# Kernel tuning notes

Hardware: AMD Instinct MI355X
Metric: run time of the kernel (lower is better)

## Reference

```python
import jax, jax.numpy as jnp
import numpy as np

HEADS = 8
HEAD_DIM = 64
GROUPS = 32
EPS = 1e-5


def setup_inputs() -> dict:
    key = jax.random.key(0)
    ks = jax.random.split(key, 8)
    B, C, H, W = 16, 256, 32, 32
    TD = 1024
    inner = HEADS * HEAD_DIM
    return {
        "x": jax.random.normal(ks[0], (B, C, H, W), jnp.float32),
        "embedding": jax.random.normal(ks[1], (B, TD), jnp.float32),
        "norm_w": jnp.ones((C,), jnp.float32),
        "norm_b": jnp.zeros((C,), jnp.float32),
        "in_w": jax.random.normal(ks[2], (3 * inner, C), jnp.float32) * (1.0 / np.sqrt(C)),
        "in_b": jnp.zeros((3 * inner,), jnp.float32),
        "out_w": jax.random.normal(ks[3], (C, inner), jnp.float32) * (1.0 / np.sqrt(inner)),
        "out_b": jnp.zeros((C,), jnp.float32),
        "emb_w": jax.random.normal(ks[4], (C, TD), jnp.float32) * (1.0 / np.sqrt(TD)),
        "emb_b": jnp.zeros((C,), jnp.float32),
    }


def reference(x, embedding, norm_w, norm_b, in_w, in_b, out_w, out_b, emb_w, emb_b):
    b, c, h, w = x.shape
    scale = 1.0 / np.sqrt(HEAD_DIM)
    # GroupNorm over (C//G, H, W) per group
    xg = x.reshape(b, GROUPS, -1)
    mean = xg.mean(-1, keepdims=True)
    var = xg.var(-1, keepdims=True)
    xn = ((xg - mean) * jax.lax.rsqrt(var + EPS)).reshape(b, c, h, w)
    xn = xn * norm_w[:, None, None] + norm_b[:, None, None]
    # 1x1 conv QKV projection: [b, 3*inner, h, w]
    qkv = jnp.einsum('oc,bchw->bohw', in_w, xn) + in_b[:, None, None]
    q, k, v = jnp.split(qkv, 3, axis=1)
    # [b, heads, head_dim, hw]
    q = q.reshape(b, HEADS, HEAD_DIM, h * w)
    k = k.reshape(b, HEADS, HEAD_DIM, h * w)
    v = v.reshape(b, HEADS, HEAD_DIM, h * w)
    attn = jax.nn.softmax(jnp.einsum('bhcm,bhcn->bhmn', q, k) * scale, axis=-1)
    o = jnp.einsum('bhmn,bhcn->bhcm', attn, v)  # [b,h,c,hw]
    o = o.reshape(b, HEADS * HEAD_DIM, h, w)
    out = jnp.einsum('oc,bchw->bohw', out_w, o) + out_b[:, None, None]
    emb = embedding @ emb_w.T + emb_b  # [b, C]
    return out * emb[:, :, None, None] + x
```

## Files before the change

kernel.cpp:

```cpp
#include <hip/hip_runtime.h>

#define DEV __device__ __forceinline__

typedef _Float16 f16;
typedef _Float16 f16x8 __attribute__((ext_vector_type(8)));
typedef _Float16 f16x4 __attribute__((ext_vector_type(4)));
typedef float f32x4 __attribute__((ext_vector_type(4)));

static constexpr int NB = 16;
static constexpr int NC = 256;
static constexpr int HW = 1024;
static constexpr int NG = 32;
static constexpr int CPG = 8;
static constexpr int NH = 8;
static constexpr int HD = 64;
static constexpr int INNER = 512;
static constexpr int TD = 1024;

DEV f32x4 mfma16(f16x8 a, f16x8 b, f32x4 c) {
    return __builtin_amdgcn_mfma_f32_16x16x32_f16(a, b, c, 0, 0, 0);
}

__global__ void gn_stats_k(const float* __restrict__ x, float* __restrict__ stats) {
    int bg = blockIdx.x;
    const float4* p = reinterpret_cast<const float4*>(x) + (size_t)bg * (CPG * HW / 4);
    float s = 0.f, ss = 0.f;
    for (int i = threadIdx.x; i < CPG * HW / 4; i += 256) {
        float4 v = p[i];
        s  += v.x + v.y + v.z + v.w;
        ss += v.x * v.x + v.y * v.y + v.z * v.z + v.w * v.w;
    }
    #pragma unroll
    for (int o = 32; o > 0; o >>= 1) {
        s  += __shfl_xor(s, o);
        ss += __shfl_xor(ss, o);
    }
    __shared__ float rs[4], rss[4];
    int wid = threadIdx.x >> 6;
    if ((threadIdx.x & 63) == 0) { rs[wid] = s; rss[wid] = ss; }
    __syncthreads();
    if (threadIdx.x == 0) {
        s  = rs[0] + rs[1] + rs[2] + rs[3];
        ss = rss[0] + rss[1] + rss[2] + rss[3];
        const float inv_n = 1.f / (float)(CPG * HW);
        float mean = s * inv_n;
        float var  = ss * inv_n - mean * mean;
        stats[bg * 2]     = mean;
        stats[bg * 2 + 1] = rsqrtf(var + 1e-5f);
    }
}

__global__ void gn_apply_k(const float* __restrict__ x, const float* __restrict__ stats,
                           const float* __restrict__ nw, const float* __restrict__ nb,
                           f16* __restrict__ xnT) {
    int b = blockIdx.y;
    int m = blockIdx.x * 256 + threadIdx.x;
    const float* xb = x + (size_t)b * NC * HW + m;
    f16* op = xnT + ((size_t)b * HW + m) * NC;
    for (int c0 = 0; c0 < NC; c0 += 4) {
        f16x4 h;
        #pragma unroll
        for (int j = 0; j < 4; ++j) {
            int c = c0 + j;
            float mean = stats[(b * NG + (c >> 3)) * 2];
            float rstd = stats[(b * NG + (c >> 3)) * 2 + 1];
            float v = xb[(size_t)c * HW];
            h[j] = (f16)(((v - mean) * rstd) * nw[c] + nb[c]);
        }
        *reinterpret_cast<f16x4*>(op + c0) = h;
    }
}

__global__ void conv_w_k(const float* __restrict__ a, const float* __restrict__ bw,
                         f16* __restrict__ wa, f16* __restrict__ wb) {
    int i = blockIdx.x * 256 + threadIdx.x;
    const int N1 = 3 * INNER * NC / 4;
    float4 v;
    f16* dst;
    if (i < N1) { v = reinterpret_cast<const float4*>(a)[i];      dst = wa + (size_t)i * 4; }
    else        { v = reinterpret_cast<const float4*>(bw)[i - N1]; dst = wb + (size_t)(i - N1) * 4; }
    f16x4 h4 = {(f16)v.x, (f16)v.y, (f16)v.z, (f16)v.w};
    *reinterpret_cast<f16x4*>(dst) = h4;
}

__global__ __launch_bounds__(256) void gemm_qkv_k(
        const f16* __restrict__ wA, const f16* __restrict__ xnT,
        const float* __restrict__ bias,
        f16* __restrict__ qT, f16* __restrict__ kT, f16* __restrict__ vv) {
    int b  = blockIdx.z;
    int o0 = blockIdx.x * 128;
    int m0 = blockIdx.y * 128;
    int wid  = threadIdx.x >> 6;
    int lane = threadIdx.x & 63;
    int wr = (wid >> 1) * 64, wc = (wid & 1) * 64;
    int lr = lane & 15, lg = lane >> 4;

    const f16* A  = wA  + (size_t)(o0 + wr + lr) * NC + lg * 8;
    const f16* Bp = xnT + ((size_t)b * HW + m0 + wc + lr) * NC + lg * 8;

    const f32x4 fzero = {0.f, 0.f, 0.f, 0.f};
    f32x4 acc[4][4];
    #pragma unroll
    for (int i = 0; i < 4; ++i) {
        #pragma unroll
        for (int j = 0; j < 4; ++j) acc[i][j] = fzero;
    }

    for (int k0 = 0; k0 < NC; k0 += 32) {
        f16x8 af[4], bf[4];
        #pragma unroll
        for (int i = 0; i < 4; ++i)
            af[i] = *reinterpret_cast<const f16x8*>(A + (size_t)i * 16 * NC + k0);
        #pragma unroll
        for (int j = 0; j < 4; ++j)
            bf[j] = *reinterpret_cast<const f16x8*>(Bp + (size_t)j * 16 * NC + k0);
        #pragma unroll
        for (int i = 0; i < 4; ++i) {
            #pragma unroll
            for (int j = 0; j < 4; ++j)
                acc[i][j] = mfma16(af[i], bf[j], acc[i][j]);
        }
    }

    #pragma unroll
    for (int i = 0; i < 4; ++i) {
        int ob = o0 + wr + i * 16 + lg * 4;
        #pragma unroll
        for (int j = 0; j < 4; ++j) {
            int m = m0 + wc + j * 16 + lr;
            float v0 = acc[i][j][0] + bias[ob];
            float v1 = acc[i][j][1] + bias[ob + 1];
            float v2 = acc[i][j][2] + bias[ob + 2];
            float v3 = acc[i][j][3] + bias[ob + 3];
            if (ob < INNER) {
                int h = ob >> 6, c = ob & 63;
                f16x4 pk = {(f16)v0, (f16)v1, (f16)v2, (f16)v3};
                *reinterpret_cast<f16x4*>(qT + (((size_t)(b * NH + h) * HW + m) * HD + c)) = pk;
            } else if (ob < 2 * INNER) {
                int oo = ob - INNER;
                int h = oo >> 6, c = oo & 63;
                f16x4 pk = {(f16)v0, (f16)v1, (f16)v2, (f16)v3};
                *reinterpret_cast<f16x4*>(kT + (((size_t)(b * NH + h) * HW + m) * HD + c)) = pk;
            } else {
                int oo = ob - 2 * INNER;
                int h = oo >> 6, c = oo & 63;
                f16* vp = vv + ((size_t)(b * NH + h) * HD + c) * HW + m;
                vp[0]      = (f16)v0;
                vp[HW]     = (f16)v1;
                vp[2 * HW] = (f16)v2;
                vp[3 * HW] = (f16)v3;
            }
        }
    }
}

__global__ void emb_gemm_k(const float* __restrict__ e, const float* __restrict__ ew,
                           const float* __restrict__ eb, float* __restrict__ embS) {
    int b = blockIdx.y;
    int co = blockIdx.x * 4 + (threadIdx.x >> 6);
    int lane = threadIdx.x & 63;
    const float4* ep = reinterpret_cast<const float4*>(e + (size_t)b * TD);
    const float4* wp = reinterpret_cast<const float4*>(ew + (size_t)co * TD);
    float s = 0.f;
    for (int t = lane; t < TD / 4; t += 64) {
        float4 a = ep[t], w = wp[t];
        s += a.x * w.x + a.y * w.y + a.z * w.z + a.w * w.w;
    }
    #pragma unroll
    for (int o = 32; o > 0; o >>= 1) s += __shfl_xor(s, o);
    if (lane == 0) embS[b * NC + co] = s + eb[co];
}

DEV void load_kv(const f16* __restrict__ kp, const f16* __restrict__ vp,
                 int n0, int lr, int lg, f16x8 (&kf)[2][2], f16x8 (&vf)[4]) {
    #pragma unroll
    for (int kt = 0; kt < 2; ++kt)
        #pragma unroll
        for (int ks2 = 0; ks2 < 2; ++ks2)
            kf[kt][ks2] = *reinterpret_cast<const f16x8*>(
                kp + (size_t)(n0 + kt * 16 + lr) * HD + ks2 * 32 + lg * 8);
    #pragma unroll
    for (int dt = 0; dt < 4; ++dt)
        vf[dt] = *reinterpret_cast<const f16x8*>(
            vp + (size_t)(dt * 16 + lr) * HW + n0 + lg * 8);
}

DEV void attn_tile(const f16x8 (&kf)[2][2], const f16x8 (&vf)[4],
                   const f16x8 (&qf)[4][2],
                   f32x4 (&oa)[4][4], float (&mr)[4], float (&lsl)[4],
                   f16 (&pl)[16][40], int lr, int lg) {
    const float sl = 0.125f * 1.44269504088896f;
    const float THR = 11.0f;
    const f32x4 fzero = {0.f, 0.f, 0.f, 0.f};
    #pragma unroll
    for (int qt = 0; qt < 4; ++qt) {
        f32x4 sc0 = fzero, sc1 = fzero;
        __builtin_amdgcn_s_setprio(1);
        sc0 = mfma16(kf[0][0], qf[qt][0], sc0);
        sc0 = mfma16(kf[0][1], qf[qt][1], sc0);
        sc1 = mfma16(kf[1][0], qf[qt][0], sc1);
        sc1 = mfma16(kf[1][1], qf[qt][1], sc1);
        __builtin_amdgcn_s_setprio(0);

        float a0 = fmaxf(fmaxf(sc0[0], sc0[1]), fmaxf(sc0[2], sc0[3]));
        float a1 = fmaxf(fmaxf(sc1[0], sc1[1]), fmaxf(sc1[2], sc1[3]));
        float pmax = fmaxf(a0, a1) * sl;
        if (__any(pmax - mr[qt] > THR)) {
            float pm = pmax;
            pm = fmaxf(pm, __shfl_xor(pm, 16));
            pm = fmaxf(pm, __shfl_xor(pm, 32));
            float mn = fmaxf(mr[qt], pm);
            float f = exp2f(mr[qt] - mn);
            mr[qt] = mn;
            lsl[qt] *= f;
            #pragma unroll
            for (int dt = 0; dt < 4; ++dt)
                #pragma unroll
                for (int r = 0; r < 4; ++r) oa[qt][dt][r] *= f;
        }
        float p[8];
        #pragma unroll
        for (int r = 0; r < 4; ++r) p[r]     = exp2f(fmaf(sc0[r], sl, -mr[qt]));
        #pragma unroll
        for (int r = 0; r < 4; ++r) p[4 + r] = exp2f(fmaf(sc1[r], sl, -mr[qt]));
        lsl[qt] += ((p[0] + p[1]) + (p[2] + p[3])) + ((p[4] + p[5]) + (p[6] + p[7]));

        f16x4 w0 = {(f16)p[0], (f16)p[1], (f16)p[2], (f16)p[3]};
        f16x4 w1 = {(f16)p[4], (f16)p[5], (f16)p[6], (f16)p[7]};
        *reinterpret_cast<f16x4*>(&pl[lr][lg * 4])      = w0;
        *reinterpret_cast<f16x4*>(&pl[lr][16 + lg * 4]) = w1;
        f16x8 pf = *reinterpret_cast<const f16x8*>(&pl[lr][lg * 8]);

        __builtin_amdgcn_s_setprio(1);
        #pragma unroll
        for (int dt = 0; dt < 4; ++dt)
            oa[qt][dt] = mfma16(vf[dt], pf, oa[qt][dt]);
        __builtin_amdgcn_s_setprio(0);
    }
}

__global__ __launch_bounds__(256) void attn_k(
        const f16* __restrict__ qT, const f16* __restrict__ kT, const f16* __restrict__ vv,
        f16* __restrict__ oT) {
    int u = ((blockIdx.x & 7) << 6) | (blockIdx.x >> 3);
    int bh = u >> 2;
    int mt = u & 3;
    int b = bh >> 3, h = bh & 7;
    int wid = threadIdx.x >> 6;
    int lane = threadIdx.x & 63;
    int lr = lane & 15, lg = lane >> 4;
    int mw = mt * 256 + wid * 64;

    const f16* qp = qT + (size_t)bh * HW * HD;
    const f16* kp = kT + (size_t)bh * HW * HD;
    const f16* vp = vv + (size_t)bh * HD * HW;

    __shared__ __align__(16) f16 pl[4][16][40];

    f16x8 qf[4][2];
    #pragma unroll
    for (int qt = 0; qt < 4; ++qt)
        #pragma unroll
        for (int ks2 = 0; ks2 < 2; ++ks2)
            qf[qt][ks2] = *reinterpret_cast<const f16x8*>(
                qp + (size_t)(mw + qt * 16 + lr) * HD + ks2 * 32 + lg * 8);

    const f32x4 fzero = {0.f, 0.f, 0.f, 0.f};
    f32x4 oa[4][4];
    #pragma unroll
    for (int qt = 0; qt < 4; ++qt)
        #pragma unroll
        for (int dt = 0; dt < 4; ++dt) oa[qt][dt] = fzero;
    float mr[4]  = {-1e30f, -1e30f, -1e30f, -1e30f};
    float lsl[4] = {0.f, 0.f, 0.f, 0.f};

    f16x8 kfA[2][2], vfA[4], kfB[2][2], vfB[4];
    load_kv(kp, vp, 0, lr, lg, kfA, vfA);
    for (int n0 = 0; n0 < HW; n0 += 64) {
        load_kv(kp, vp, n0 + 32, lr, lg, kfB, vfB);
        attn_tile(kfA, vfA, qf, oa, mr, lsl, pl[wid], lr, lg);
        if (n0 + 64 < HW) load_kv(kp, vp, n0 + 64, lr, lg, kfA, vfA);
        attn_tile(kfB, vfB, qf, oa, mr, lsl, pl[wid], lr, lg);
    }

    #pragma unroll
    for (int qt = 0; qt < 4; ++qt) {
        float t = lsl[qt];
        t += __shfl_xor(t, 16);
        t += __shfl_xor(t, 32);
        float inv = 1.f / t;
        int m = mw + qt * 16 + lr;
        f16* op = oT + ((size_t)b * HW + m) * INNER + h * HD;
        #pragma unroll
        for (int dt = 0; dt < 4; ++dt) {
            f16x4 o4;
            #pragma unroll
            for (int r = 0; r < 4; ++r) o4[r] = (f16)(oa[qt][dt][r] * inv);
            *reinterpret_cast<f16x4*>(op + dt * 16 + lg * 4) = o4;
        }
    }
}

__global__ __launch_bounds__(256) void gemm_out_k(
        const f16* __restrict__ wA, const f16* __restrict__ oT,
        const float* __restrict__ bias, const float* __restrict__ embS,
        const float* __restrict__ x, float* __restrict__ out) {
    int b  = blockIdx.z;
    int o0 = blockIdx.x * 128;
    int m0 = blockIdx.y * 128;
    int wid  = threadIdx.x >> 6;
    int lane = threadIdx.x & 63;
    int wr = (wid >> 1) * 64, wc = (wid & 1) * 64;
    int lr = lane & 15, lg = lane >> 4;

    const f16* A  = wA + (size_t)(o0 + wr + lr) * INNER + lg * 8;
    const f16* Bp = oT + ((size_t)b * HW + m0 + wc + lr) * INNER + lg * 8;

    const f32x4 fzero = {0.f, 0.f, 0.f, 0.f};
    f32x4 acc[4][4];
    #pragma unroll
    for (int i = 0; i < 4; ++i) {
        #pragma unroll
        for (int j = 0; j < 4; ++j) acc[i][j] = fzero;
    }

    for (int k0 = 0; k0 < INNER; k0 += 32) {
        f16x8 af[4], bf[4];
        #pragma unroll
        for (int i = 0; i < 4; ++i)
            af[i] = *reinterpret_cast<const f16x8*>(A + (size_t)i * 16 * INNER + k0);
        #pragma unroll
        for (int j = 0; j < 4; ++j)
            bf[j] = *reinterpret_cast<const f16x8*>(Bp + (size_t)j * 16 * INNER + k0);
        #pragma unroll
        for (int i = 0; i < 4; ++i) {
            #pragma unroll
            for (int j = 0; j < 4; ++j)
                acc[i][j] = mfma16(af[i], bf[j], acc[i][j]);
        }
    }

    #pragma unroll
    for (int i = 0; i < 4; ++i) {
        int ob = o0 + wr + i * 16 + lg * 4;
        #pragma unroll
        for (int j = 0; j < 4; ++j) {
            int m = m0 + wc + j * 16 + lr;
            #pragma unroll
            for (int r = 0; r < 4; ++r) {
                int o = ob + r;
                size_t idx = ((size_t)b * NC + o) * HW + m;
                out[idx] = (acc[i][j][r] + bias[o]) * embS[b * NC + o] + x[idx];
            }
        }
    }
}

extern "C" void kernel_launch(void* const* d_in, const int* in_sizes, int n_in,
                              void* d_out, int out_size, void* d_ws, size_t ws_size,
                              hipStream_t stream) {
    const float* x     = (const float*)d_in[0];
    const float* emb   = (const float*)d_in[1];
    const float* nw    = (const float*)d_in[2];
    const float* nbi   = (const float*)d_in[3];
    const float* in_w  = (const float*)d_in[4];
    const float* in_b  = (const float*)d_in[5];
    const float* out_w = (const float*)d_in[6];
    const float* out_b = (const float*)d_in[7];
    const float* emb_w = (const float*)d_in[8];
    const float* emb_b = (const float*)d_in[9];

    char* p = (char*)d_ws;
    f16* xnT   = (f16*)p;   p += (size_t)NB * HW * NC * 2;
    f16* w_in  = (f16*)p;   p += (size_t)3 * INNER * NC * 2;
    f16* w_out = (f16*)p;   p += (size_t)NC * INNER * 2;
    float* stats = (float*)p; p += (size_t)NB * NG * 2 * 4;
    float* embS  = (float*)p; p += (size_t)NB * NC * 4;
    f16* qT = (f16*)p;      p += (size_t)NB * NH * HW * HD * 2;
    f16* kT = (f16*)p;      p += (size_t)NB * NH * HW * HD * 2;
    f16* vv = (f16*)p;      p += (size_t)NB * NH * HW * HD * 2;
    f16* oT = (f16*)p;

    gn_stats_k<<<NB * NG, 256, 0, stream>>>(x, stats);
    gn_apply_k<<<dim3(HW / 256, NB), 256, 0, stream>>>(x, stats, nw, nbi, xnT);
    conv_w_k<<<512, 256, 0, stream>>>(in_w, out_w, w_in, w_out);
    gemm_qkv_k<<<dim3(12, 8, NB), 256, 0, stream>>>(w_in, xnT, in_b, qT, kT, vv);
    emb_gemm_k<<<dim3(NC / 4, NB), 256, 0, stream>>>(emb, emb_w, emb_b, embS);
    attn_k<<<512, 256, 0, stream>>>(qT, kT, vv, oT);
    gemm_out_k<<<dim3(NC / 128, HW / 128, NB), 256, 0, stream>>>(w_out, oT, out_b, embS, x, (float*)d_out);
}
```

Baseline: 178.4 us.

## Fuse prep kernels, fold softmax scale into K, remap GEMM grids

Merges the GroupNorm stats, weight conversion and embedding GEMM into one launch to cut launch overhead and let independent work overlap. Folds the softmax scale and log2e into K when the QKV GEMM writes it, which removes a multiply per score in attention, and packs probabilities with cvt_pkrtz. The QKV and output GEMMs get a 1D grid with a swizzled block order for better cache locality. The output GEMM uses smaller 64-row tiles for more blocks, and gn_apply is reorganised to write 8-wide vectors across more blocks. K is now stored pre-scaled in fp16, which slightly changes rounding.

```diff
diff --git a/kernel.cpp b/kernel.cpp
--- a/kernel.cpp
+++ b/kernel.cpp
@@ -6,6 +6,7 @@
 typedef _Float16 f16x8 __attribute__((ext_vector_type(8)));
 typedef _Float16 f16x4 __attribute__((ext_vector_type(4)));
 typedef float f32x4 __attribute__((ext_vector_type(4)));
+typedef unsigned int u32;
 
 static constexpr int NB = 16;
 static constexpr int NC = 256;
@@ -21,32 +22,69 @@
     return __builtin_amdgcn_mfma_f32_16x16x32_f16(a, b, c, 0, 0, 0);
 }
 
-__global__ void gn_stats_k(const float* __restrict__ x, float* __restrict__ stats) {
-    int bg = blockIdx.x;
-    const float4* p = reinterpret_cast<const float4*>(x) + (size_t)bg * (CPG * HW / 4);
-    float s = 0.f, ss = 0.f;
-    for (int i = threadIdx.x; i < CPG * HW / 4; i += 256) {
-        float4 v = p[i];
-        s  += v.x + v.y + v.z + v.w;
-        ss += v.x * v.x + v.y * v.y + v.z * v.z + v.w * v.w;
-    }
-    #pragma unroll
-    for (int o = 32; o > 0; o >>= 1) {
-        s  += __shfl_xor(s, o);
-        ss += __shfl_xor(ss, o);
-    }
-    __shared__ float rs[4], rss[4];
-    int wid = threadIdx.x >> 6;
-    if ((threadIdx.x & 63) == 0) { rs[wid] = s; rss[wid] = ss; }
-    __syncthreads();
-    if (threadIdx.x == 0) {
-        s  = rs[0] + rs[1] + rs[2] + rs[3];
-        ss = rss[0] + rss[1] + rss[2] + rss[3];
-        const float inv_n = 1.f / (float)(CPG * HW);
-        float mean = s * inv_n;
-        float var  = ss * inv_n - mean * mean;
-        stats[bg * 2]     = mean;
-        stats[bg * 2 + 1] = rsqrtf(var + 1e-5f);
+DEV u32 pk2(float a, float b) {
+    auto c = __builtin_amdgcn_cvt_pkrtz(a, b);
+    return __builtin_bit_cast(u32, c);
+}
+struct u32x2 { u32 a, b; };
+
+__global__ void prep_k(const float* __restrict__ x, float* __restrict__ stats,
+                       const float* __restrict__ in_w, const float* __restrict__ out_w,
+                       f16* __restrict__ w_in, f16* __restrict__ w_out,
+                       const float* __restrict__ e, const float* __restrict__ ew,
+                       const float* __restrict__ eb, float* __restrict__ embS) {
+    int bid = blockIdx.x;
+    if (bid < NB * NG) {
+        int bg = bid;
+        const float4* p = reinterpret_cast<const float4*>(x) + (size_t)bg * (CPG * HW / 4);
+        float s = 0.f, ss = 0.f;
+        for (int i = threadIdx.x; i < CPG * HW / 4; i += 256) {
+            float4 v = p[i];
+            s  += v.x + v.y + v.z + v.w;
+            ss += v.x * v.x + v.y * v.y + v.z * v.z + v.w * v.w;
+        }
+        #pragma unroll
+        for (int o = 32; o > 0; o >>= 1) {
+            s  += __shfl_xor(s, o);
+            ss += __shfl_xor(ss, o);
+        }
+        __shared__ float rs[4], rss[4];
+        int wid = threadIdx.x >> 6;
+        if ((threadIdx.x & 63) == 0) { rs[wid] = s; rss[wid] = ss; }
+        __syncthreads();
+        if (threadIdx.x == 0) {
+            s  = rs[0] + rs[1] + rs[2] + rs[3];
+            ss = rss[0] + rss[1] + rss[2] + rss[3];
+            const float inv_n = 1.f / (float)(CPG * HW);
+            float mean = s * inv_n;
+            float var  = ss * inv_n - mean * mean;
+            stats[bg * 2]     = mean;
+            stats[bg * 2 + 1] = rsqrtf(var + 1e-5f);
+        }
+    } else if (bid < NB * NG + 512) {
+        int i = (bid - NB * NG) * 256 + threadIdx.x;
+        const int N1 = 3 * INNER * NC / 4;
+        float4 v;
+        f16* dst;
+        if (i < N1) { v = reinterpret_cast<const float4*>(in_w)[i];       dst = w_in + (size_t)i * 4; }
+        else        { v = reinterpret_cast<const float4*>(out_w)[i - N1]; dst = w_out + (size_t)(i - N1) * 4; }
+        f16x4 h4 = {(f16)v.x, (f16)v.y, (f16)v.z, (f16)v.w};
+        *reinterpret_cast<f16x4*>(dst) = h4;
+    } else {
+        int u = bid - (NB * NG + 512);
+        int b = u >> 6;
+        int co = ((u & 63) << 2) + (threadIdx.x >> 6);
+        int lane = threadIdx.x & 63;
+        const float4* ep = reinterpret_cast<const float4*>(e + (size_t)b * TD);
+        const float4* wp = reinterpret_cast<const float4*>(ew + (size_t)co * TD);
+        float s = 0.f;
+        for (int t = lane; t < TD / 4; t += 64) {
+            float4 a = ep[t], w = wp[t];
+            s += a.x * w.x + a.y * w.y + a.z * w.z + a.w * w.w;
+        }
+        #pragma unroll
+        for (int o = 32; o > 0; o >>= 1) s += __shfl_xor(s, o);
+        if (lane == 0) embS[b * NC + co] = s + eb[co];
     }
 }
 
@@ -54,42 +92,36 @@
                            const float* __restrict__ nw, const float* __restrict__ nb,
                            f16* __restrict__ xnT) {
     int b = blockIdx.y;
-    int m = blockIdx.x * 256 + threadIdx.x;
+    int m = blockIdx.x * 64 + (threadIdx.x & 63);
+    int c0 = (threadIdx.x >> 6) * 64;
     const float* xb = x + (size_t)b * NC * HW + m;
-    f16* op = xnT + ((size_t)b * HW + m) * NC;
-    for (int c0 = 0; c0 < NC; c0 += 4) {
-        f16x4 h;
-        #pragma unroll
-        for (int j = 0; j < 4; ++j) {
-            int c = c0 + j;
-            float mean = stats[(b * NG + (c >> 3)) * 2];
-            float rstd = stats[(b * NG + (c >> 3)) * 2 + 1];
+    f16* op = xnT + ((size_t)b * HW + m) * NC + c0;
+    #pragma unroll
+    for (int cc = 0; cc < 64; cc += 8) {
+        int cg = c0 + cc;
+        float mean = stats[(b * NG + (cg >> 3)) * 2];
+        float rstd = stats[(b * NG + (cg >> 3)) * 2 + 1];
+        f16x8 h;
+        #pragma unroll
+        for (int j = 0; j < 8; ++j) {
+            int c = cg + j;
             float v = xb[(size_t)c * HW];
             h[j] = (f16)(((v - mean) * rstd) * nw[c] + nb[c]);
         }
-        *reinterpret_cast<f16x4*>(op + c0) = h;
-    }
-}
-
-__global__ void conv_w_k(const float* __restrict__ a, const float* __restrict__ bw,
-                         f16* __restrict__ wa, f16* __restrict__ wb) {
-    int i = blockIdx.x * 256 + threadIdx.x;
-    const int N1 = 3 * INNER * NC / 4;
-    float4 v;
-    f16* dst;
-    if (i < N1) { v = reinterpret_cast<const float4*>(a)[i];      dst = wa + (size_t)i * 4; }
-    else        { v = reinterpret_cast<const float4*>(bw)[i - N1]; dst = wb + (size_t)(i - N1) * 4; }
-    f16x4 h4 = {(f16)v.x, (f16)v.y, (f16)v.z, (f16)v.w};
-    *reinterpret_cast<f16x4*>(dst) = h4;
+        *reinterpret_cast<f16x8*>(op + cc) = h;
+    }
 }
 
 __global__ __launch_bounds__(256) void gemm_qkv_k(
         const f16* __restrict__ wA, const f16* __restrict__ xnT,
         const float* __restrict__ bias,
         f16* __restrict__ qT, f16* __restrict__ kT, f16* __restrict__ vv) {
-    int b  = blockIdx.z;
-    int o0 = blockIdx.x * 128;
-    int m0 = blockIdx.y * 128;
+    int bid = blockIdx.x;
+    int u = (bid & 7) * 192 + (bid >> 3);
+    int o0 = (u % 12) * 128;
+    int rr = u / 12;
+    int m0 = (rr & 7) * 128;
+    int b  = rr >> 3;
     int wid  = threadIdx.x >> 6;
     int lane = threadIdx.x & 63;
     int wr = (wid >> 1) * 64, wc = (wid & 1) * 64;
@@ -122,6 +154,7 @@
         }
     }
 
+    const float SL = 0.18033688011112042f;
     #pragma unroll
     for (int i = 0; i < 4; ++i) {
         int ob = o0 + wr + i * 16 + lg * 4;
@@ -139,7 +172,7 @@
             } else if (ob < 2 * INNER) {
                 int oo = ob - INNER;
                 int h = oo >> 6, c = oo & 63;
-                f16x4 pk = {(f16)v0, (f16)v1, (f16)v2, (f16)v3};
+                f16x4 pk = {(f16)(v0 * SL), (f16)(v1 * SL), (f16)(v2 * SL), (f16)(v3 * SL)};
                 *reinterpret_cast<f16x4*>(kT + (((size_t)(b * NH + h) * HW + m) * HD + c)) = pk;
             } else {
                 int oo = ob - 2 * INNER;
@@ -154,23 +187,6 @@
     }
 }
 
-__global__ void emb_gemm_k(const float* __restrict__ e, const float* __restrict__ ew,
-                           const float* __restrict__ eb, float* __restrict__ embS) {
-    int b = blockIdx.y;
-    int co = blockIdx.x * 4 + (threadIdx.x >> 6);
-    int lane = threadIdx.x & 63;
-    const float4* ep = reinterpret_cast<const float4*>(e + (size_t)b * TD);
-    const float4* wp = reinterpret_cast<const float4*>(ew + (size_t)co * TD);
-    float s = 0.f;
-    for (int t = lane; t < TD / 4; t += 64) {
-        float4 a = ep[t], w = wp[t];
-        s += a.x * w.x + a.y * w.y + a.z * w.z + a.w * w.w;
-    }
-    #pragma unroll
-    for (int o = 32; o > 0; o >>= 1) s += __shfl_xor(s, o);
-    if (lane == 0) embS[b * NC + co] = s + eb[co];
-}
-
 DEV void load_kv(const f16* __restrict__ kp, const f16* __restrict__ vp,
                  int n0, int lr, int lg, f16x8 (&kf)[2][2], f16x8 (&vf)[4]) {
     #pragma unroll
@@ -189,7 +205,6 @@
                    const f16x8 (&qf)[4][2],
                    f32x4 (&oa)[4][4], float (&mr)[4], float (&lsl)[4],
                    f16 (&pl)[16][40], int lr, int lg) {
-    const float sl = 0.125f * 1.44269504088896f;
     const float THR = 11.0f;
     const f32x4 fzero = {0.f, 0.f, 0.f, 0.f};
     #pragma unroll
@@ -202,9 +217,9 @@
         sc1 = mfma16(kf[1][1], qf[qt][1], sc1);
         __builtin_amdgcn_s_setprio(0);
 
-        float a0 = fmaxf(fmaxf(sc0[0], sc0[1]), fmaxf(sc0[2], sc0[3]));
-        float a1 = fmaxf(fmaxf(sc1[0], sc1[1]), fmaxf(sc1[2], sc1[3]));
-        float pmax = fmaxf(a0, a1) * sl;
+        float m0 = fmaxf(fmaxf(sc0[0], sc0[1]), fmaxf(sc0[2], sc0[3]));
+        float m1 = fmaxf(fmaxf(sc1[0], sc1[1]), fmaxf(sc1[2], sc1[3]));
+        float pmax = fmaxf(m0, m1);
         if (__any(pmax - mr[qt] > THR)) {
             float pm = pmax;
             pm = fmaxf(pm, __shfl_xor(pm, 16));
@@ -220,15 +235,15 @@
         }
         float p[8];
         #pragma unroll
-        for (int r = 0; r < 4; ++r) p[r]     = exp2f(fmaf(sc0[r], sl, -mr[qt]));
-        #pragma unroll
-        for (int r = 0; r < 4; ++r) p[4 + r] = exp2f(fmaf(sc1[r], sl, -mr[qt]));
+        for (int r = 0; r < 4; ++r) p[r]     = exp2f(sc0[r] - mr[qt]);
+        #pragma unroll
+        for (int r = 0; r < 4; ++r) p[4 + r] = exp2f(sc1[r] - mr[qt]);
         lsl[qt] += ((p[0] + p[1]) + (p[2] + p[3])) + ((p[4] + p[5]) + (p[6] + p[7]));
 
-        f16x4 w0 = {(f16)p[0], (f16)p[1], (f16)p[2], (f16)p[3]};
-        f16x4 w1 = {(f16)p[4], (f16)p[5], (f16)p[6], (f16)p[7]};
-        *reinterpret_cast<f16x4*>(&pl[lr][lg * 4])      = w0;
-        *reinterpret_cast<f16x4*>(&pl[lr][16 + lg * 4]) = w1;
+        u32x2 wlo = {pk2(p[0], p[1]), pk2(p[2], p[3])};
+        u32x2 whi = {pk2(p[4], p[5]), pk2(p[6], p[7])};
+        *reinterpret_cast<u32x2*>(&pl[lr][lg * 4])      = wlo;
+        *reinterpret_cast<u32x2*>(&pl[lr][16 + lg * 4]) = whi;
         f16x8 pf = *reinterpret_cast<const f16x8*>(&pl[lr][lg * 8]);
 
         __builtin_amdgcn_s_setprio(1);
@@ -305,35 +320,38 @@
         const f16* __restrict__ wA, const f16* __restrict__ oT,
         const float* __restrict__ bias, const float* __restrict__ embS,
         const float* __restrict__ x, float* __restrict__ out) {
-    int b  = blockIdx.z;
-    int o0 = blockIdx.x * 128;
-    int m0 = blockIdx.y * 128;
+    int bid = blockIdx.x;
+    int u = (bid & 7) * 64 + (bid >> 3);
+    int o0 = (u & 3) * 64;
+    int rr = u >> 2;
+    int m0 = (rr & 7) * 128;
+    int b  = rr >> 3;
     int wid  = threadIdx.x >> 6;
     int lane = threadIdx.x & 63;
-    int wr = (wid >> 1) * 64, wc = (wid & 1) * 64;
+    int wr = (wid >> 1) * 32, wc = (wid & 1) * 64;
     int lr = lane & 15, lg = lane >> 4;
 
     const f16* A  = wA + (size_t)(o0 + wr + lr) * INNER + lg * 8;
     const f16* Bp = oT + ((size_t)b * HW + m0 + wc + lr) * INNER + lg * 8;
 
     const f32x4 fzero = {0.f, 0.f, 0.f, 0.f};
-    f32x4 acc[4][4];
-    #pragma unroll
-    for (int i = 0; i < 4; ++i) {
+    f32x4 acc[2][4];
+    #pragma unroll
+    for (int i = 0; i < 2; ++i) {
         #pragma unroll
         for (int j = 0; j < 4; ++j) acc[i][j] = fzero;
     }
 
     for (int k0 = 0; k0 < INNER; k0 += 32) {
-        f16x8 af[4], bf[4];
-        #pragma unroll
-        for (int i = 0; i < 4; ++i)
+        f16x8 af[2], bf[4];
+        #pragma unroll
+        for (int i = 0; i < 2; ++i)
             af[i] = *reinterpret_cast<const f16x8*>(A + (size_t)i * 16 * INNER + k0);
         #pragma unroll
         for (int j = 0; j < 4; ++j)
             bf[j] = *reinterpret_cast<const f16x8*>(Bp + (size_t)j * 16 * INNER + k0);
         #pragma unroll
-        for (int i = 0; i < 4; ++i) {
+        for (int i = 0; i < 2; ++i) {
             #pragma unroll
             for (int j = 0; j < 4; ++j)
                 acc[i][j] = mfma16(af[i], bf[j], acc[i][j]);
@@ -341,7 +359,7 @@
     }
 
     #pragma unroll
-    for (int i = 0; i < 4; ++i) {
+    for (int i = 0; i < 2; ++i) {
         int ob = o0 + wr + i * 16 + lg * 4;
         #pragma unroll
         for (int j = 0; j < 4; ++j) {
@@ -381,11 +399,10 @@
     f16* vv = (f16*)p;      p += (size_t)NB * NH * HW * HD * 2;
     f16* oT = (f16*)p;
 
-    gn_stats_k<<<NB * NG, 256, 0, stream>>>(x, stats);
-    gn_apply_k<<<dim3(HW / 256, NB), 256, 0, stream>>>(x, stats, nw, nbi, xnT);
-    conv_w_k<<<512, 256, 0, stream>>>(in_w, out_w, w_in, w_out);
-    gemm_qkv_k<<<dim3(12, 8, NB), 256, 0, stream>>>(w_in, xnT, in_b, qT, kT, vv);
-    emb_gemm_k<<<dim3(NC / 4, NB), 256, 0, stream>>>(emb, emb_w, emb_b, embS);
+    prep_k<<<NB * NG + 512 + 1024, 256, 0, stream>>>(x, stats, in_w, out_w, w_in, w_out,
+                                                     emb, emb_w, emb_b, embS);
+    gn_apply_k<<<dim3(HW / 64, NB), 256, 0, stream>>>(x, stats, nw, nbi, xnT);
+    gemm_qkv_k<<<1536, 256, 0, stream>>>(w_in, xnT, in_b, qT, kT, vv);
     attn_k<<<512, 256, 0, stream>>>(qT, kT, vv, oT);
-    gemm_out_k<<<dim3(NC / 128, HW / 128, NB), 256, 0, stream>>>(w_out, oT, out_b, embS, x, (float*)d_out);
-}
+    gemm_out_k<<<512, 256, 0, stream>>>(w_out, oT, out_b, embS, x, (float*)d_out);
+}
```

New measurement: 170.5 us. 4.4% less time.
